# Kernel tuning notes

Hardware: AMD Instinct MI355X
Metric: run time of the kernel (lower is better)

The kernel has to match this reference:

```python
import jax, jax.numpy as jnp
import numpy as np


def setup_inputs() -> dict:
    key = jax.random.key(0)
    ks = jax.random.split(key, 7)
    B = 4096
    x = jax.random.normal(ks[0], (B, 1, 28, 28), dtype=jnp.float32)
    # conv1: Conv2d(1, 32, 3), conv2: Conv2d(32, 64, 3)
    w1 = jax.random.normal(ks[1], (32, 1, 3, 3), dtype=jnp.float32) * 0.1
    b1 = jax.random.normal(ks[2], (32,), dtype=jnp.float32) * 0.1
    w2 = jax.random.normal(ks[3], (64, 32, 3, 3), dtype=jnp.float32) * 0.05
    b2 = jax.random.normal(ks[4], (64,), dtype=jnp.float32) * 0.05
    # fc1: Linear(9216, 128), fc2: Linear(128, 10)
    fc1_w = jax.random.normal(ks[5], (128, 9216), dtype=jnp.float32) * 0.01
    fc1_b = jnp.zeros((128,), dtype=jnp.float32)
    fc2_w = jax.random.normal(ks[6], (10, 128), dtype=jnp.float32) * 0.05
    fc2_b = jnp.zeros((10,), dtype=jnp.float32)
    return {"x": x, "w1": w1, "b1": b1, "w2": w2, "b2": b2,
            "fc1_w": fc1_w, "fc1_b": fc1_b, "fc2_w": fc2_w, "fc2_b": fc2_b}


def _conv_valid(x, w, b):
    # The original FFTConv1d (flatten-to-1D FFT circular correlation + roll +
    # crop) is mathematically identical to valid cross-correlation (nn.Conv2d).
    y = jax.lax.conv_general_dilated(
        x, w, window_strides=(1, 1), padding="VALID",
        dimension_numbers=("NCHW", "OIHW", "NCHW"))
    return y + b[None, :, None, None]


def reference(x, w1, b1, w2, b2, fc1_w, fc1_b, fc2_w, fc2_b):
    h = jax.nn.relu(_conv_valid(x, w1, b1))        # [B,32,26,26]
    h = jax.nn.relu(_conv_valid(h, w2, b2))        # [B,64,24,24]
    B, C, H, W = h.shape
    h = h.reshape(B, C, H // 2, 2, W // 2, 2).max(axis=(3, 5))  # maxpool 2x2 -> [B,64,12,12]
    # dropout layers are identity at inference
    h = h.reshape(B, -1)                           # [B,9216], C-major like torch.flatten
    h = jax.nn.relu(h @ fc1_w.T + fc1_b)           # [B,128]
    logits = h @ fc2_w.T + fc2_b                   # [B,10]
    # original computes log_softmax but returns the pre-softmax logits
    return logits
```

## Files before the change

kernel.cpp:

```cpp
#include <hip/hip_runtime.h>
#include <hip/hip_bf16.h>
#include <string.h>

using short8 = __attribute__((ext_vector_type(8))) short;
using f32x4  = __attribute__((ext_vector_type(4))) float;
using f32x2  = __attribute__((ext_vector_type(2))) float;

#define POOLN     9216
#define FC1N      128
#define WT2_ELEMS 18432
#define WT2_BYTES 36864
#define H1S_STRIDE 36

#define GLL16(gp, lp) __builtin_amdgcn_global_load_lds( \
    (const __attribute__((address_space(1))) void*)(gp), \
    (__attribute__((address_space(3))) void*)(lp), 16, 0, 0)

static __device__ __forceinline__ unsigned short f2bf(float f) {
  unsigned int u = __builtin_bit_cast(unsigned int, f);
  unsigned int r = (u + 0x7FFFu + ((u >> 16) & 1u)) >> 16;
  return (unsigned short)r;
}

static __device__ __forceinline__ unsigned int pkbf(float lo, float hi) {
  __hip_bfloat162 h2 = __float22bfloat162_rn(make_float2(lo, hi));
  unsigned int r;
  memcpy(&r, &h2, sizeof(r));
  return r;
}

__global__ __launch_bounds__(256) void k_wt2(const float* __restrict__ w2,
    unsigned short* __restrict__ wt2) {
  int idx = blockIdx.x * 256 + threadIdx.x;
  if (idx >= WT2_ELEMS) return;
  int j = idx & 7;
  int l = (idx >> 3) & 63;
  int tn = idx >> 9;
  int tap = tn >> 2, n = tn & 3;
  int oc = n * 16 + (l & 15);
  int ic = (l >> 4) * 8 + j;
  wt2[idx] = f2bf(w2[oc * 288 + ic * 9 + tap]);
}

__global__ __launch_bounds__(256) void k_fw1t(const float* __restrict__ w,
    unsigned short* __restrict__ wt) {
  int c = blockIdx.x;
  __shared__ float row[9216];
  int t = threadIdx.x;
  const float* src = w + (size_t)c * 9216;
  for (int i = t; i < 9216; i += 256) row[i] = src[i];
  __syncthreads();
  unsigned short* dst = wt + (size_t)c * 9216;
  for (int k = t; k < 9216; k += 256) {
    int sp = k >> 6, oc = k & 63;
    dst[k] = f2bf(row[oc * 144 + sp]);
  }
}

__global__ __launch_bounds__(512, 4) void kc_fused(const float* __restrict__ x,
    const float* __restrict__ w1, const float* __restrict__ b1,
    const unsigned short* __restrict__ wt2, const float* __restrict__ b2,
    unsigned short* __restrict__ pooled) {
  int img = blockIdx.x;
  int tt = blockIdx.y;
  __shared__ __align__(16) unsigned short h1s[260 * H1S_STRIDE];
  __shared__ __align__(16) unsigned short wlds[WT2_ELEMS];
  int t = threadIdx.x;
  int wv = t >> 6, ln = t & 63;
  int r0x = tt * 8;

  {
    const char* gw = (const char*)wt2 + ln * 16;
    char* wb = (char*)wlds;
    #pragma unroll
    for (int i = 0; i < 5; ++i) {
      int cc = wv + i * 8;
      if (cc < 36) GLL16(gw + cc * 1024, wb + cc * 1024);
    }
  }

  int wvu = __builtin_amdgcn_readfirstlane(wv);
  f32x2 wp[2][9], bp[2];
  #pragma unroll
  for (int p = 0; p < 2; ++p) {
    int o = wvu * 4 + p * 2;
    bp[p] = (f32x2){b1[o], b1[o + 1]};
    #pragma unroll
    for (int q = 0; q < 9; ++q)
      wp[p][q] = (f32x2){w1[o * 9 + q], w1[(o + 1) * 9 + q]};
  }

  if (ln < 52) {
    int half = (ln >= 26);
    int xcol = ln - half * 26;
    int y0 = half * 5;
    const float* xg = x + (size_t)img * 784 + (size_t)(r0x + y0) * 28 + xcol;
    float win[3][3];
    #pragma unroll
    for (int c = 0; c < 3; ++c) {
      win[1][c] = xg[c];
      win[2][c] = xg[28 + c];
    }
    #pragma unroll
    for (int i = 0; i < 5; ++i) {
      #pragma unroll
      for (int c = 0; c < 3; ++c) {
        win[0][c] = win[1][c];
        win[1][c] = win[2][c];
        win[2][c] = xg[(i + 2) * 28 + c];
      }
      f32x2 s[2] = {bp[0], bp[1]};
      #pragma unroll
      for (int r = 0; r < 3; ++r)
        #pragma unroll
        for (int c = 0; c < 3; ++c) {
          f32x2 wv2 = (f32x2){win[r][c], win[r][c]};
          #pragma unroll
          for (int p = 0; p < 2; ++p)
            s[p] = __builtin_elementwise_fma(wv2, wp[p][r * 3 + c], s[p]);
        }
      unsigned int packed[2];
      const f32x2 z2 = (f32x2){0.f, 0.f};
      #pragma unroll
      for (int p = 0; p < 2; ++p) {
        f32x2 sp = __builtin_elementwise_max(s[p], z2);
        packed[p] = pkbf(sp.x, sp.y);
      }
      int pos = (y0 + i) * 26 + xcol;
      unsigned short* dst = &h1s[pos * H1S_STRIDE + wvu * 4];
      *(uint2*)dst = make_uint2(packed[0], packed[1]);
    }
  }
  __syncthreads();

  int col = ln & 15;
  int g = (ln >> 4) & 3;
  int mr = wv >> 1;
  int nh = wv & 1;

  int abase[3];
  #pragma unroll
  for (int i = 0; i < 3; ++i) {
    int y = 2 * mr + (col & 1);
    int xx = 8 * i + (col >> 1);
    abase[i] = (y * 26 + xx) * (H1S_STRIDE * 2) + g * 16;
  }

  f32x4 acc[3][2];
  #pragma unroll
  for (int m = 0; m < 3; ++m)
    #pragma unroll
    for (int n = 0; n < 2; ++n)
      acc[m][n] = (f32x4){0.f, 0.f, 0.f, 0.f};

  const char* hsb = (const char*)h1s;
  const char* wb = (const char*)wlds;
  #pragma unroll
  for (int tap = 0; tap < 9; ++tap) {
    int ky = tap / 3, kx = tap - ky * 3;
    int toff = (ky * 26 + kx) * (H1S_STRIDE * 2);
    short8 bf[2];
    #pragma unroll
    for (int n = 0; n < 2; ++n)
      bf[n] = *(const short8*)(wb + (tap * 4 + nh * 2 + n) * 1024 + ln * 16);
    #pragma unroll
    for (int m = 0; m < 3; ++m) {
      union { short8 v; uint2 d[2]; } af;
      af.d[0] = *(const uint2*)(hsb + abase[m] + toff);
      af.d[1] = *(const uint2*)(hsb + abase[m] + toff + 8);
      #pragma unroll
      for (int n = 0; n < 2; ++n)
        acc[m][n] = __builtin_amdgcn_mfma_f32_16x16x32_bf16(af.v, bf[n], acc[m][n], 0, 0, 0);
    }
  }

  float bias[2];
  #pragma unroll
  for (int n = 0; n < 2; ++n) bias[n] = b2[(nh * 2 + n) * 16 + col];
  unsigned short* pp = pooled + (size_t)img * POOLN;
  int pr = tt * 4 + mr;
  #pragma unroll
  for (int m = 0; m < 3; ++m) {
    int sp = pr * 12 + m * 4 + g;
    float rv[2];
    #pragma unroll
    for (int n = 0; n < 2; ++n) {
      f32x4 a = acc[m][n];
      float v = fmaxf(fmaxf(a[0], a[1]), fmaxf(a[2], a[3]));
      rv[n] = fmaxf(v + bias[n], 0.f);
    }
    unsigned int p01 = pkbf(rv[0], rv[1]);
    unsigned short* pr0 = pp + sp * 64 + nh * 32 + col;
    pr0[0]  = (unsigned short)p01;
    pr0[16] = (unsigned short)(p01 >> 16);
  }
}

__global__ __launch_bounds__(256) void k3_fc1_mfma(
    const unsigned short* __restrict__ a, const unsigned short* __restrict__ w,
    float* __restrict__ part, int nrpad) {
  __shared__ __align__(16) unsigned short As[2][4096];
  __shared__ __align__(16) unsigned short Bs[2][8192];
  int row0 = blockIdx.x * 64;
  int kbase = blockIdx.y * 2304;
  int t = threadIdx.x;
  int wv = t >> 6, l = t & 63;
  int rsub = l >> 3;
  int src_sw = ((l & 7) ^ rsub) << 4;

  const char* abase = (const char*)a + (size_t)row0 * 18432;
  const char* bbase = (const char*)w;

  auto stage = [&](int buf, int step) {
    size_t k0b = (size_t)(kbase + step * 64) * 2;
    #pragma unroll
    for (int i = 0; i < 2; ++i) {
      int c = wv * 2 + i;
      GLL16(abase + (size_t)(c * 8 + rsub) * 18432 + k0b + src_sw,
            (char*)As[buf] + c * 1024);
    }
    #pragma unroll
    for (int i = 0; i < 4; ++i) {
      int c = wv * 4 + i;
      GLL16(bbase + (size_t)(c * 8 + rsub) * 18432 + k0b + src_sw,
            (char*)Bs[buf] + c * 1024);
    }
  };

  int wm = wv >> 1, wn = wv & 1;
  int lr = l & 15, g2 = l >> 4;
  int rdxor = (lr & 7) << 4;

  f32x4 acc[2][4];
  #pragma unroll
  for (int mf = 0; mf < 2; ++mf)
    #pragma unroll
    for (int nf = 0; nf < 4; ++nf)
      acc[mf][nf] = (f32x4){0.f, 0.f, 0.f, 0.f};

  stage(0, 0);
  __syncthreads();
  for (int s = 0; s < 36; ++s) {
    int cur = s & 1;
    if (s < 35) stage(cur ^ 1, s + 1);
    const char* Ab = (const char*)As[cur];
    const char* Bb = (const char*)Bs[cur];
    #pragma unroll
    for (int ksub = 0; ksub < 2; ++ksub) {
      int koff = (ksub * 64 + g2 * 16) ^ rdxor;
      short8 af0 = *(const short8*)(Ab + (wm * 32 + lr) * 128 + koff);
      short8 af1 = *(const short8*)(Ab + (wm * 32 + 16 + lr) * 128 + koff);
      short8 bf[4];
      #pragma unroll
      for (int nf = 0; nf < 4; ++nf)
        bf[nf] = *(const short8*)(Bb + (wn * 64 + nf * 16 + lr) * 128 + koff);
      #pragma unroll
      for (int nf = 0; nf < 4; ++nf) {
        acc[0][nf] = __builtin_amdgcn_mfma_f32_16x16x32_bf16(af0, bf[nf], acc[0][nf], 0, 0, 0);
        acc[1][nf] = __builtin_amdgcn_mfma_f32_16x16x32_bf16(af1, bf[nf], acc[1][nf], 0, 0, 0);
      }
    }
    __syncthreads();
  }

  float* pp = part + (size_t)blockIdx.y * nrpad * 128 + (size_t)row0 * 128;
  #pragma unroll
  for (int mf = 0; mf < 2; ++mf)
    #pragma unroll
    for (int nf = 0; nf < 4; ++nf)
      #pragma unroll
      for (int rr = 0; rr < 4; ++rr) {
        int r = wm * 32 + mf * 16 + g2 * 4 + rr;
        int c = wn * 64 + nf * 16 + lr;
        pp[r * 128 + c] = acc[mf][nf][rr];
      }
}

__global__ __launch_bounds__(256) void k_tail(const float* __restrict__ part,
    const float* __restrict__ fb1, const float* __restrict__ fw2,
    const float* __restrict__ fb2, float* __restrict__ out,
    int nr, int nrpad) {
  __shared__ float sh[2][128];
  int t = threadIdx.x;
  int r = t >> 7, c = t & 127;
  int row = blockIdx.x * 2 + r;
  size_t stride = (size_t)nrpad * 128;
  if (row < nr) {
    size_t i = (size_t)row * 128 + c;
    float s = part[i] + part[stride + i] + part[2 * stride + i] + part[3 * stride + i];
    sh[r][c] = fmaxf(s + fb1[c], 0.f);
  }
  __syncthreads();
  if (t < 20) {
    int rr = t / 10, j = t - rr * 10;
    int orow = blockIdx.x * 2 + rr;
    if (orow < nr) {
      const float4* hv = (const float4*)sh[rr];
      const float4* wv = (const float4*)(fw2 + (size_t)j * 128);
      float s = 0.f;
      #pragma unroll
      for (int q = 0; q < 32; ++q) {
        float4 h4 = hv[q];
        float4 w4 = wv[q];
        s = fmaf(h4.x, w4.x, s);
        s = fmaf(h4.y, w4.y, s);
        s = fmaf(h4.z, w4.z, s);
        s = fmaf(h4.w, w4.w, s);
      }
      out[(size_t)orow * 10 + j] = s + fb2[j];
    }
  }
}

extern "C" void kernel_launch(void* const* d_in, const int* in_sizes, int n_in,
                              void* d_out, int out_size, void* d_ws, size_t ws_size,
                              hipStream_t stream) {
  const float* x   = (const float*)d_in[0];
  const float* w1  = (const float*)d_in[1];
  const float* b1  = (const float*)d_in[2];
  const float* w2  = (const float*)d_in[3];
  const float* b2  = (const float*)d_in[4];
  const float* fw1 = (const float*)d_in[5];
  const float* fb1 = (const float*)d_in[6];
  const float* fw2 = (const float*)d_in[7];
  const float* fb2 = (const float*)d_in[8];
  float* out = (float*)d_out;

  const int B = in_sizes[0] / 784;

  unsigned short* wt2 = (unsigned short*)d_ws;
  unsigned short* fw1t = (unsigned short*)((char*)d_ws + WT2_BYTES);
  const size_t carve = WT2_BYTES + (size_t)9216 * 128 * 2;
  char* base = (char*)d_ws + carve;
  size_t avail = (ws_size > carve) ? ws_size - carve : 0;
  const size_t per_img = (size_t)POOLN * 2 + 2048;
  int Bc = (int)(avail / per_img);
  if (Bc > B) Bc = B;
  Bc &= ~63;
  if (Bc < 64) Bc = 64;

  unsigned short* pooled = (unsigned short*)base;
  float* part = (float*)(base + (size_t)Bc * (POOLN * 2));

  k_wt2<<<(WT2_ELEMS + 255) / 256, 256, 0, stream>>>(w2, wt2);
  k_fw1t<<<128, 256, 0, stream>>>(fw1, fw1t);

  for (int i0 = 0; i0 < B; i0 += Bc) {
    int nr = (B - i0 < Bc) ? (B - i0) : Bc;
    int mtiles = (nr + 63) / 64;
    int nrpad = mtiles * 64;
    kc_fused<<<dim3(nr, 3), 512, 0, stream>>>(x + (size_t)i0 * 784, w1, b1,
                                              wt2, b2, pooled);
    k3_fc1_mfma<<<dim3(mtiles, 4), 256, 0, stream>>>(pooled, fw1t, part, nrpad);
    k_tail<<<(nr + 1) / 2, 256, 0, stream>>>(part, fb1, fw2, fb2,
                                             out + (size_t)i0 * 10, nr, nrpad);
  }
}
```

Measured before the change: 171.6 us.

## Process four images per block with double-buffered conv1/conv2 software pipeline

The fused conv kernel now handles four images per block, computing conv1 of the next image into a second LDS buffer while conv2 runs on the current one. The conv2 weights are no longer staged in LDS and are read directly from global memory, cutting LDS use so the double buffer fits. The intent is to overlap conv1 VALU work with MFMA work and to amortise per-block setup across images. The risks are fewer blocks in the grid, repeated global or L2 weight reads each tap, and the assumption that nr is divisible by IPB.

After: 171.0 us. No clear change (-0.4%).

```diff
diff --git a/kernel.cpp b/kernel.cpp
--- a/kernel.cpp
+++ b/kernel.cpp
@@ -11,6 +11,7 @@
 #define WT2_ELEMS 18432
 #define WT2_BYTES 36864
 #define H1S_STRIDE 36
+#define IPB       4
 
 #define GLL16(gp, lp) __builtin_amdgcn_global_load_lds( \
     (const __attribute__((address_space(1))) void*)(gp), \
@@ -57,28 +58,17 @@
   }
 }
 
-__global__ __launch_bounds__(512, 4) void kc_fused(const float* __restrict__ x,
+__global__ __launch_bounds__(512, 4) void kc_pipe(const float* __restrict__ x,
     const float* __restrict__ w1, const float* __restrict__ b1,
     const unsigned short* __restrict__ wt2, const float* __restrict__ b2,
     unsigned short* __restrict__ pooled) {
-  int img = blockIdx.x;
+  int g0 = blockIdx.x * IPB;
   int tt = blockIdx.y;
-  __shared__ __align__(16) unsigned short h1s[260 * H1S_STRIDE];
-  __shared__ __align__(16) unsigned short wlds[WT2_ELEMS];
+  __shared__ __align__(16) unsigned short h1s[2][260 * H1S_STRIDE];
   int t = threadIdx.x;
   int wv = t >> 6, ln = t & 63;
   int r0x = tt * 8;
 
-  {
-    const char* gw = (const char*)wt2 + ln * 16;
-    char* wb = (char*)wlds;
-    #pragma unroll
-    for (int i = 0; i < 5; ++i) {
-      int cc = wv + i * 8;
-      if (cc < 36) GLL16(gw + cc * 1024, wb + cc * 1024);
-    }
-  }
-
   int wvu = __builtin_amdgcn_readfirstlane(wv);
   f32x2 wp[2][9], bp[2];
   #pragma unroll
@@ -90,10 +80,28 @@
       wp[p][q] = (f32x2){w1[o * 9 + q], w1[(o + 1) * 9 + q]};
   }
 
-  if (ln < 52) {
-    int half = (ln >= 26);
-    int xcol = ln - half * 26;
-    int y0 = half * 5;
+  int half = (ln >= 26);
+  int xcol = ln - half * 26;
+  if (xcol > 25) xcol = 25;
+  bool c1act = (ln < 52);
+  int y0 = half * 5;
+
+  int col = ln & 15;
+  int g = (ln >> 4) & 3;
+  int mr = wv >> 1;
+  int nh = wv & 1;
+  int abase[3];
+  #pragma unroll
+  for (int i = 0; i < 3; ++i) {
+    int y = 2 * mr + (col & 1);
+    int xx = 8 * i + (col >> 1);
+    abase[i] = (y * 26 + xx) * (H1S_STRIDE * 2) + g * 16;
+  }
+  float bias[2];
+  #pragma unroll
+  for (int n = 0; n < 2; ++n) bias[n] = b2[(nh * 2 + n) * 16 + col];
+
+  auto conv1_body = [&](int img, int buf) {
     const float* xg = x + (size_t)img * 784 + (size_t)(r0x + y0) * 28 + xcol;
     float win[3][3];
     #pragma unroll
@@ -126,73 +134,66 @@
         f32x2 sp = __builtin_elementwise_max(s[p], z2);
         packed[p] = pkbf(sp.x, sp.y);
       }
-      int pos = (y0 + i) * 26 + xcol;
-      unsigned short* dst = &h1s[pos * H1S_STRIDE + wvu * 4];
-      *(uint2*)dst = make_uint2(packed[0], packed[1]);
-    }
-  }
+      if (c1act) {
+        int pos = (y0 + i) * 26 + xcol;
+        unsigned short* dst = &h1s[buf][pos * H1S_STRIDE + wvu * 4];
+        *(uint2*)dst = make_uint2(packed[0], packed[1]);
+      }
+    }
+  };
+
+  auto conv2_body = [&](int img, int buf) {
+    const char* hsb = (const char*)h1s[buf];
+    f32x4 acc[3][2];
+    #pragma unroll
+    for (int m = 0; m < 3; ++m)
+      #pragma unroll
+      for (int n = 0; n < 2; ++n)
+        acc[m][n] = (f32x4){0.f, 0.f, 0.f, 0.f};
+    #pragma unroll
+    for (int tap = 0; tap < 9; ++tap) {
+      int ky = tap / 3, kx = tap - ky * 3;
+      int toff = (ky * 26 + kx) * (H1S_STRIDE * 2);
+      short8 bf[2];
+      #pragma unroll
+      for (int n = 0; n < 2; ++n)
+        bf[n] = *(const short8*)(wt2 + ((size_t)(tap * 4 + nh * 2 + n) * 64 + ln) * 8);
+      #pragma unroll
+      for (int m = 0; m < 3; ++m) {
+        union { short8 v; uint2 d[2]; } af;
+        af.d[0] = *(const uint2*)(hsb + abase[m] + toff);
+        af.d[1] = *(const uint2*)(hsb + abase[m] + toff + 8);
+        #pragma unroll
+        for (int n = 0; n < 2; ++n)
+          acc[m][n] = __builtin_amdgcn_mfma_f32_16x16x32_bf16(af.v, bf[n], acc[m][n], 0, 0, 0);
+      }
+    }
+    unsigned short* pp = pooled + (size_t)img * POOLN;
+    int pr = tt * 4 + mr;
+    #pragma unroll
+    for (int m = 0; m < 3; ++m) {
+      int sp = pr * 12 + m * 4 + g;
+      float rv[2];
+      #pragma unroll
+      for (int n = 0; n < 2; ++n) {
+        f32x4 a = acc[m][n];
+        float v = fmaxf(fmaxf(a[0], a[1]), fmaxf(a[2], a[3]));
+        rv[n] = fmaxf(v + bias[n], 0.f);
+      }
+      unsigned int p01 = pkbf(rv[0], rv[1]);
+      unsigned short* pr0 = pp + sp * 64 + nh * 32 + col;
+      pr0[0]  = (unsigned short)p01;
+      pr0[16] = (unsigned short)(p01 >> 16);
+    }
+  };
+
+  conv1_body(g0, 0);
   __syncthreads();
-
-  int col = ln & 15;
-  int g = (ln >> 4) & 3;
-  int mr = wv >> 1;
-  int nh = wv & 1;
-
-  int abase[3];
-  #pragma unroll
-  for (int i = 0; i < 3; ++i) {
-    int y = 2 * mr + (col & 1);
-    int xx = 8 * i + (col >> 1);
-    abase[i] = (y * 26 + xx) * (H1S_STRIDE * 2) + g * 16;
-  }
-
-  f32x4 acc[3][2];
-  #pragma unroll
-  for (int m = 0; m < 3; ++m)
-    #pragma unroll
-    for (int n = 0; n < 2; ++n)
-      acc[m][n] = (f32x4){0.f, 0.f, 0.f, 0.f};
-
-  const char* hsb = (const char*)h1s;
-  const char* wb = (const char*)wlds;
-  #pragma unroll
-  for (int tap = 0; tap < 9; ++tap) {
-    int ky = tap / 3, kx = tap - ky * 3;
-    int toff = (ky * 26 + kx) * (H1S_STRIDE * 2);
-    short8 bf[2];
-    #pragma unroll
-    for (int n = 0; n < 2; ++n)
-      bf[n] = *(const short8*)(wb + (tap * 4 + nh * 2 + n) * 1024 + ln * 16);
-    #pragma unroll
-    for (int m = 0; m < 3; ++m) {
-      union { short8 v; uint2 d[2]; } af;
-      af.d[0] = *(const uint2*)(hsb + abase[m] + toff);
-      af.d[1] = *(const uint2*)(hsb + abase[m] + toff + 8);
-      #pragma unroll
-      for (int n = 0; n < 2; ++n)
-        acc[m][n] = __builtin_amdgcn_mfma_f32_16x16x32_bf16(af.v, bf[n], acc[m][n], 0, 0, 0);
-    }
-  }
-
-  float bias[2];
-  #pragma unroll
-  for (int n = 0; n < 2; ++n) bias[n] = b2[(nh * 2 + n) * 16 + col];
-  unsigned short* pp = pooled + (size_t)img * POOLN;
-  int pr = tt * 4 + mr;
-  #pragma unroll
-  for (int m = 0; m < 3; ++m) {
-    int sp = pr * 12 + m * 4 + g;
-    float rv[2];
-    #pragma unroll
-    for (int n = 0; n < 2; ++n) {
-      f32x4 a = acc[m][n];
-      float v = fmaxf(fmaxf(a[0], a[1]), fmaxf(a[2], a[3]));
-      rv[n] = fmaxf(v + bias[n], 0.f);
-    }
-    unsigned int p01 = pkbf(rv[0], rv[1]);
-    unsigned short* pr0 = pp + sp * 64 + nh * 32 + col;
-    pr0[0]  = (unsigned short)p01;
-    pr0[16] = (unsigned short)(p01 >> 16);
+  #pragma unroll
+  for (int p = 0; p < IPB; ++p) {
+    if (p + 1 < IPB) conv1_body(g0 + p + 1, (p + 1) & 1);
+    conv2_body(g0 + p, p & 1);
+    __syncthreads();
   }
 }
 
@@ -349,8 +350,8 @@
     int nr = (B - i0 < Bc) ? (B - i0) : Bc;
     int mtiles = (nr + 63) / 64;
     int nrpad = mtiles * 64;
-    kc_fused<<<dim3(nr, 3), 512, 0, stream>>>(x + (size_t)i0 * 784, w1, b1,
-                                              wt2, b2, pooled);
+    kc_pipe<<<dim3(nr / IPB, 3), 512, 0, stream>>>(x + (size_t)i0 * 784, w1, b1,
+                                                   wt2, b2, pooled);
     k3_fc1_mfma<<<dim3(mtiles, 4), 256, 0, stream>>>(pooled, fw1t, part, nrpad);
     k_tail<<<(nr + 1) / 2, 256, 0, stream>>>(part, fb1, fw2, fb2,
                                              out + (size_t)i0 * 10, nr, nrpad);
```
